# Kernel tuning notes

Measured on AMD Instinct MI355X. Metric: run time of the kernel, lower is better.

The kernel has to match this reference:

```python
import jax, jax.numpy as jnp
import numpy as np

NUM_NODES, FEAT_DIM, DIM, CLIPS = 100000, 128, 128, 8
S1, S2 = 10, 10
B, L = 1024, 8


def setup_inputs() -> dict:
    key = jax.random.key(0)
    k1, k2, k3, k4, k5 = jax.random.split(key, 5)
    features = jax.random.normal(k1, (NUM_NODES, FEAT_DIM), dtype=jnp.float32)
    # xavier-uniform-ish init for the per-clip projection
    local_weight = jax.random.normal(k2, (CLIPS, DIM, FEAT_DIM), dtype=jnp.float32) * (2.0 / (DIM + FEAT_DIM)) ** 0.5
    nodes = jax.random.randint(k3, (B, L), 0, NUM_NODES, dtype=jnp.int64 if jax.config.jax_enable_x64 else jnp.int32)
    neigh1 = jax.random.randint(k4, (NUM_NODES, S1), 0, NUM_NODES, dtype=nodes.dtype)
    neigh2 = jax.random.randint(k5, (NUM_NODES, S2), 0, NUM_NODES, dtype=nodes.dtype)
    return {"features": features, "local_weight": local_weight, "nodes": nodes,
            "neigh1": neigh1, "neigh2": neigh2}


def reference(features, local_weight, nodes, neigh1, neigh2):
    b, l = nodes.shape
    nf = nodes.reshape(-1)                     # [N] flat nodes
    # hop-0: raw features
    feat_self = features[nf]                   # [N, d]
    # hop-1: mean over sampled 1-hop neighbors (agg1)
    feats1 = features[neigh1[nf]].mean(axis=1)  # [N, s1, d] -> [N, d]
    # hop-2: mean over sampled 2-hop neighbors of agg1 outputs (agg2)
    two_hop = neigh1[neigh2[nf]]               # [N, s2, s1]
    feats2 = features[two_hop].mean(axis=2).mean(axis=1)  # [N, d]
    # per-clip projection: einsum('ckd,dn->ckn').permute(2,0,1) == 'ckd,nd->nck'
    outs = [jnp.einsum('ckd,nd->nck', local_weight, f)
            for f in (feats1, feats2, feat_self)]         # each [N, clips, dim]
    local = jnp.concatenate(outs, axis=-1)                # [N, clips, 3*dim]
    local = local.reshape(b, l, local_weight.shape[0], -1)
    return jax.nn.relu(local)
```

## Files before the change

kernel.cpp:

```cpp
#include <hip/hip_runtime.h>

typedef __attribute__((ext_vector_type(8))) short bf16x8;
typedef __attribute__((ext_vector_type(4))) float f32x4;

static constexpr int N_NODES = 8192;
static constexpr int FEAT    = 128;
static constexpr int NB      = 16;
static constexpr int NBLK    = N_NODES / NB;
static constexpr int XS      = 136;
static constexpr int FEAT_BLOCKS = 6250;

__device__ __forceinline__ unsigned short f2bf(float f) {
    unsigned u = __builtin_bit_cast(unsigned, f);
    u += 0x7FFFu + ((u >> 16) & 1u);
    return (unsigned short)(u >> 16);
}
__device__ __forceinline__ float bf2f(unsigned short h) {
    return __builtin_bit_cast(float, ((unsigned)h) << 16);
}
__device__ __forceinline__ void acc8(float* a, const uint4 v) {
    a[0] += bf2f((unsigned short)(v.x & 0xffffu));
    a[1] += bf2f((unsigned short)(v.x >> 16));
    a[2] += bf2f((unsigned short)(v.y & 0xffffu));
    a[3] += bf2f((unsigned short)(v.y >> 16));
    a[4] += bf2f((unsigned short)(v.z & 0xffffu));
    a[5] += bf2f((unsigned short)(v.z >> 16));
    a[6] += bf2f((unsigned short)(v.w & 0xffffu));
    a[7] += bf2f((unsigned short)(v.w >> 16));
}
__device__ __forceinline__ uint4 pack8(const float* a, float sc) {
    uint4 o;
    o.x = (unsigned)f2bf(a[0] * sc) | ((unsigned)f2bf(a[1] * sc) << 16);
    o.y = (unsigned)f2bf(a[2] * sc) | ((unsigned)f2bf(a[3] * sc) << 16);
    o.z = (unsigned)f2bf(a[4] * sc) | ((unsigned)f2bf(a[5] * sc) << 16);
    o.w = (unsigned)f2bf(a[6] * sc) | ((unsigned)f2bf(a[7] * sc) << 16);
    return o;
}

__global__ void __launch_bounds__(256) pack_all(
    const float* __restrict__ feat, const float* __restrict__ lw,
    unsigned short* __restrict__ T, unsigned short* __restrict__ Wp)
{
    const int b = blockIdx.x;
    if (b < FEAT_BLOCKS) {
        const size_t i = (size_t)b * 256 + threadIdx.x;
        const f32x4* src = (const f32x4*)feat;
        const f32x4 v0 = __builtin_nontemporal_load(src + i * 2);
        const f32x4 v1 = __builtin_nontemporal_load(src + i * 2 + 1);
        ushort4 o0, o1;
        o0.x = f2bf(v0[0]); o0.y = f2bf(v0[1]); o0.z = f2bf(v0[2]); o0.w = f2bf(v0[3]);
        o1.x = f2bf(v1[0]); o1.y = f2bf(v1[1]); o1.z = f2bf(v1[2]); o1.w = f2bf(v1[3]);
        ((ushort4*)T)[i * 2]     = o0;
        ((ushort4*)T)[i * 2 + 1] = o1;
    } else {
        const int i = (b - FEAT_BLOCKS) * 256 + threadIdx.x;
        const float4 v = ((const float4*)lw)[i];
        ushort4 o;
        o.x = f2bf(v.x); o.y = f2bf(v.y); o.z = f2bf(v.z); o.w = f2bf(v.w);
        ((ushort4*)Wp)[i] = o;
    }
}

__global__ void __launch_bounds__(256) fused_enc(
    const unsigned short* __restrict__ T,
    const int*   __restrict__ nodes,
    const int*   __restrict__ n1,
    const int*   __restrict__ n2,
    const unsigned short* __restrict__ Wp,
    float* __restrict__ out)
{
    __shared__ int nfs[NB];
    __shared__ int sm_m[NB][10];
    __shared__ int idx[NB][112];
    __shared__ unsigned short X[3 * NB][XS];

    const int blk = blockIdx.x;
    const int tid = threadIdx.x;

    if (tid < NB) nfs[tid] = nodes[blk * NB + tid];
    __syncthreads();
    if (tid < NB * 10) {
        const int i = tid / 10, s = tid - (tid / 10) * 10;
        idx[i][s] = n1[nfs[i] * 10 + s];
    }
    if (tid >= 96) {
        const int t = tid - 96;
        const int i = t / 10, s = t - (t / 10) * 10;
        sm_m[i][s] = n2[nfs[i] * 10 + s];
    }
    if (tid < NB) idx[tid][110] = nfs[tid];
    __syncthreads();
    for (int t = tid; t < NB * 100; t += 256) {
        const int i = t / 100, rr = t - (t / 100) * 100;
        idx[i][10 + rr] = n1[sm_m[i][rr / 10] * 10 + (rr - (rr / 10) * 10)];
    }
    __syncthreads();

    {
        const int g = tid >> 4;
        const int l = tid & 15;
        const unsigned short* Tl = T + l * 8;

        float aA[8] = {0,0,0,0,0,0,0,0};
        float aB[8] = {0,0,0,0,0,0,0,0};
        uint4 v[10];

#pragma unroll
        for (int s = 0; s < 10; ++s) v[s] = *(const uint4*)(Tl + (size_t)idx[g][s] * FEAT);
#pragma unroll
        for (int s = 0; s < 10; ++s) acc8(aA, v[s]);
#pragma unroll
        for (int c = 1; c <= 10; ++c) {
#pragma unroll
            for (int s = 0; s < 10; ++s)
                v[s] = *(const uint4*)(Tl + (size_t)idx[g][c * 10 + s] * FEAT);
#pragma unroll
            for (int s = 0; s < 10; ++s) acc8(aB, v[s]);
        }
        const uint4 sv = *(const uint4*)(Tl + (size_t)idx[g][110] * FEAT);
        *(uint4*)&X[g * 3 + 2][l * 8] = sv;
        *(uint4*)&X[g * 3 + 0][l * 8] = pack8(aA, 0.1f);
        *(uint4*)&X[g * 3 + 1][l * 8] = pack8(aB, 0.01f);
    }
    __syncthreads();

    const int wave = tid >> 6;
    const int lane = tid & 63;
    const int r = lane & 15;
    const int q = lane >> 4;

#pragma unroll
    for (int ch = 0; ch < 4; ++ch) {
        const int yBase = wave * 256 + ch * 64;
        f32x4 acc[3][4];
#pragma unroll
        for (int mt = 0; mt < 3; ++mt)
#pragma unroll
            for (int nj = 0; nj < 4; ++nj) acc[mt][nj] = (f32x4){0.f, 0.f, 0.f, 0.f};

#pragma unroll
        for (int k0 = 0; k0 < 4; ++k0) {
            bf16x8 a[3], b[4];
#pragma unroll
            for (int mt = 0; mt < 3; ++mt)
                a[mt] = *(const bf16x8*)&X[mt * 16 + r][k0 * 32 + q * 8];
#pragma unroll
            for (int nj = 0; nj < 4; ++nj)
                b[nj] = *(const bf16x8*)(Wp + (size_t)(yBase + nj * 16 + r) * FEAT
                                            + q * 8 + k0 * 32);
#pragma unroll
            for (int mt = 0; mt < 3; ++mt)
#pragma unroll
                for (int nj = 0; nj < 4; ++nj)
                    acc[mt][nj] = __builtin_amdgcn_mfma_f32_16x16x32_bf16(
                        a[mt], b[nj], acc[mt][nj], 0, 0, 0);
        }

#pragma unroll
        for (int mt = 0; mt < 3; ++mt) {
#pragma unroll
            for (int i = 0; i < 4; ++i) {
                const int xl = mt * 16 + q * 4 + i;
                const int nl = xl / 3;
                const int j  = xl - nl * 3;
                float* orow = out + (size_t)(blk * NB + nl) * 3072 + j * 128;
#pragma unroll
                for (int nj = 0; nj < 4; ++nj) {
                    const int y = yBase + nj * 16 + r;
                    const int c = y >> 7;
                    const int k = y & 127;
                    orow[c * 384 + k] = fmaxf(acc[mt][nj][i], 0.f);
                }
            }
        }
    }
}

extern "C" void kernel_launch(void* const* d_in, const int* in_sizes, int n_in,
                              void* d_out, int out_size, void* d_ws, size_t ws_size,
                              hipStream_t stream) {
    const float* features = (const float*)d_in[0];
    const float* lw       = (const float*)d_in[1];
    const int*   nodes    = (const int*)d_in[2];
    const int*   n1       = (const int*)d_in[3];
    const int*   n2       = (const int*)d_in[4];
    float*       out      = (float*)d_out;

    unsigned short* Wp = (unsigned short*)d_ws;
    unsigned short* T  = Wp + (size_t)1024 * FEAT;

    pack_all<<<FEAT_BLOCKS + 128, 256, 0, stream>>>(features, lw, T, Wp);
    fused_enc<<<NBLK, 256, 0, stream>>>(T, nodes, n1, n2, Wp, out);
}
```

Baseline: 72.72 us.

## Double fused_enc block to 512 threads, splitting gather and GEMM work

The fused encoder block grows from 256 to 512 threads. Each node's 110-row gather is split across two 16-lane groups, and their partial sums are reduced through a new shared-memory buffer. The MFMA projection is spread over 8 waves with half the output columns each. The aim is more memory-level parallelism for the latency-bound random gathers and shorter per-wave projection loops. The cost is extra shared memory, an added barrier, an imbalanced split (one half also does hop-1 and the self load) and possibly lower block occupancy.

After: 78.62 us. 1.08x slower.

```diff
diff --git a/kernel.cpp b/kernel.cpp
--- a/kernel.cpp
+++ b/kernel.cpp
@@ -61,7 +61,7 @@
     }
 }
 
-__global__ void __launch_bounds__(256) fused_enc(
+__global__ void __launch_bounds__(512) fused_enc(
     const unsigned short* __restrict__ T,
     const int*   __restrict__ nodes,
     const int*   __restrict__ n1,
@@ -73,54 +73,77 @@
     __shared__ int sm_m[NB][10];
     __shared__ int idx[NB][112];
     __shared__ unsigned short X[3 * NB][XS];
+    __shared__ float red[NB][FEAT];
 
     const int blk = blockIdx.x;
     const int tid = threadIdx.x;
 
     if (tid < NB) nfs[tid] = nodes[blk * NB + tid];
     __syncthreads();
-    if (tid < NB * 10) {
+    if (tid < 160) {
         const int i = tid / 10, s = tid - (tid / 10) * 10;
         idx[i][s] = n1[nfs[i] * 10 + s];
-    }
-    if (tid >= 96) {
-        const int t = tid - 96;
+    } else if (tid < 320) {
+        const int t = tid - 160;
         const int i = t / 10, s = t - (t / 10) * 10;
         sm_m[i][s] = n2[nfs[i] * 10 + s];
-    }
-    if (tid < NB) idx[tid][110] = nfs[tid];
-    __syncthreads();
-    for (int t = tid; t < NB * 100; t += 256) {
+    } else if (tid < 320 + NB) {
+        idx[tid - 320][110] = nfs[tid - 320];
+    }
+    __syncthreads();
+    for (int t = tid; t < NB * 100; t += 512) {
         const int i = t / 100, rr = t - (t / 100) * 100;
         idx[i][10 + rr] = n1[sm_m[i][rr / 10] * 10 + (rr - (rr / 10) * 10)];
     }
     __syncthreads();
 
     {
-        const int g = tid >> 4;
-        const int l = tid & 15;
+        const int grp  = tid >> 4;
+        const int node = grp >> 1;
+        const int half = grp & 1;
+        const int l    = tid & 15;
         const unsigned short* Tl = T + l * 8;
 
         float aA[8] = {0,0,0,0,0,0,0,0};
         float aB[8] = {0,0,0,0,0,0,0,0};
         uint4 v[10];
 
-#pragma unroll
-        for (int s = 0; s < 10; ++s) v[s] = *(const uint4*)(Tl + (size_t)idx[g][s] * FEAT);
-#pragma unroll
-        for (int s = 0; s < 10; ++s) acc8(aA, v[s]);
-#pragma unroll
-        for (int c = 1; c <= 10; ++c) {
+        if (!half) {
 #pragma unroll
             for (int s = 0; s < 10; ++s)
-                v[s] = *(const uint4*)(Tl + (size_t)idx[g][c * 10 + s] * FEAT);
-#pragma unroll
-            for (int s = 0; s < 10; ++s) acc8(aB, v[s]);
-        }
-        const uint4 sv = *(const uint4*)(Tl + (size_t)idx[g][110] * FEAT);
-        *(uint4*)&X[g * 3 + 2][l * 8] = sv;
-        *(uint4*)&X[g * 3 + 0][l * 8] = pack8(aA, 0.1f);
-        *(uint4*)&X[g * 3 + 1][l * 8] = pack8(aB, 0.01f);
+                v[s] = *(const uint4*)(Tl + (size_t)idx[node][s] * FEAT);
+#pragma unroll
+            for (int s = 0; s < 10; ++s) acc8(aA, v[s]);
+#pragma unroll
+            for (int c = 1; c <= 5; ++c) {
+#pragma unroll
+                for (int s = 0; s < 10; ++s)
+                    v[s] = *(const uint4*)(Tl + (size_t)idx[node][c * 10 + s] * FEAT);
+#pragma unroll
+                for (int s = 0; s < 10; ++s) acc8(aB, v[s]);
+            }
+        } else {
+#pragma unroll
+            for (int c = 6; c <= 10; ++c) {
+#pragma unroll
+                for (int s = 0; s < 10; ++s)
+                    v[s] = *(const uint4*)(Tl + (size_t)idx[node][c * 10 + s] * FEAT);
+#pragma unroll
+                for (int s = 0; s < 10; ++s) acc8(aB, v[s]);
+            }
+#pragma unroll
+            for (int h = 0; h < 2; ++h)
+                *(f32x4*)&red[node][l * 8 + h * 4] = *(const f32x4*)&aB[h * 4];
+        }
+        __syncthreads();
+        if (!half) {
+            const uint4 sv = *(const uint4*)(Tl + (size_t)idx[node][110] * FEAT);
+#pragma unroll
+            for (int h = 0; h < 8; ++h) aB[h] += red[node][l * 8 + h];
+            *(uint4*)&X[node * 3 + 2][l * 8] = sv;
+            *(uint4*)&X[node * 3 + 0][l * 8] = pack8(aA, 0.1f);
+            *(uint4*)&X[node * 3 + 1][l * 8] = pack8(aB, 0.01f);
+        }
     }
     __syncthreads();
 
@@ -130,8 +153,8 @@
     const int q = lane >> 4;
 
 #pragma unroll
-    for (int ch = 0; ch < 4; ++ch) {
-        const int yBase = wave * 256 + ch * 64;
+    for (int ch = 0; ch < 2; ++ch) {
+        const int yBase = wave * 128 + ch * 64;
         f32x4 acc[3][4];
 #pragma unroll
         for (int mt = 0; mt < 3; ++mt)
@@ -190,5 +213,5 @@
     unsigned short* T  = Wp + (size_t)1024 * FEAT;
 
     pack_all<<<FEAT_BLOCKS + 128, 256, 0, stream>>>(features, lw, T, Wp);
-    fused_enc<<<NBLK, 256, 0, stream>>>(T, nodes, n1, n2, Wp, out);
-}
+    fused_enc<<<NBLK, 512, 0, stream>>>(T, nodes, n1, n2, Wp, out);
+}
```
